# Performance work log

Measured on AMD Instinct MI355X. Metric: run time of the kernel, lower is better.

## Reference

```python
import jax, jax.numpy as jnp
import numpy as np

N, T0, T1, C = 65536, 128, 64, 16
MIN_NEAR = 0.05


def _searchsorted(a, v):
    # batched right-side searchsorted over last dim
    return jax.vmap(lambda aa, vv: jnp.searchsorted(aa, vv, side='right'))(a, v)


def contract(x):
    # MERF-style contraction, x: [..., 3]
    ax = jnp.abs(x)
    mag = jnp.max(ax, axis=-1, keepdims=True)              # [..., 1]
    idx = jnp.argmax(ax, axis=-1)                          # [...]
    oh = jnp.arange(x.shape[-1]) == idx[..., None]         # one-hot of max axis
    inv = 1.0 / mag
    scale = jnp.where(oh, (2.0 - inv) * inv, inv)
    return jnp.where(mag < 1.0, x, x * scale)


def sample_pdf(bins, weights, T):
    # bins: [N, T0+1], weights: [N, T0] -> new bins [N, T]
    n, t0 = weights.shape
    w = weights + 0.01
    pdf = w / jnp.sum(w, -1, keepdims=True)
    cdf = jnp.minimum(jnp.cumsum(pdf, -1), 1.0)
    cdf = jnp.concatenate([jnp.zeros_like(cdf[..., :1]), cdf], -1)  # [N, T0+1]
    u = jnp.linspace(0.5 / T, 1.0 - 0.5 / T, T, dtype=bins.dtype)
    u = jnp.broadcast_to(u, (n, T))
    inds = _searchsorted(cdf, u)
    below = jnp.clip(inds - 1, 0, t0)
    above = jnp.clip(inds, 0, t0)
    g = lambda a, i: jnp.take_along_axis(a, i, axis=-1)
    cdf0, cdf1 = g(cdf, below), g(cdf, above)
    b0, b1 = g(bins, below), g(bins, above)
    t = jnp.clip(jnp.nan_to_num((u - cdf0) / (cdf1 - cdf0)), 0.0, 1.0)
    return b0 + t * (b1 - b0)


def compute_weights(real_bins, sigmas):
    deltas = real_bins[..., 1:] - real_bins[..., :-1]
    ds = deltas * sigmas
    alphas = 1.0 - jnp.exp(-ds)
    trans = jnp.exp(-jnp.concatenate(
        [jnp.zeros_like(ds[..., :1]), jnp.cumsum(ds[..., :-1], -1)], -1))
    return jnp.nan_to_num(alphas * trans)


def loss_interlevel(t0, w0, t1, w1):
    cw1 = jnp.concatenate([jnp.zeros_like(w1[..., :1]), jnp.cumsum(w1, -1)], -1)
    hi_clip = w1.shape[-1] - 1
    inds_lo = jnp.clip(_searchsorted(t1[..., :-1], t0[..., :-1]) - 1, 0, hi_clip)
    inds_hi = jnp.clip(_searchsorted(t1[..., 1:], t0[..., 1:]), 0, hi_clip)
    cw1_lo = jnp.take_along_axis(cw1[..., :-1], inds_lo, axis=-1)
    cw1_hi = jnp.take_along_axis(cw1[..., 1:], inds_hi, axis=-1)
    w = cw1_hi - cw1_lo
    return jnp.maximum(w0 - w, 0.0) ** 2 / (w0 + 1e-8)


def eff_distloss(w, m, interval):
    # efficient O(T) distortion loss (torch_efficient_distloss)
    loss_uni = (1.0 / 3.0) * jnp.mean(jnp.sum(interval * w ** 2, -1))
    wm = w * m
    w_cs = jnp.cumsum(w, -1)
    wm_cs = jnp.cumsum(wm, -1)
    loss_bi = 2.0 * jnp.mean(jnp.sum(
        wm[..., 1:] * w_cs[..., :-1] - w[..., 1:] * wm_cs[..., :-1], -1))
    return loss_uni + loss_bi


def setup_inputs():
    key = jax.random.key(0)
    ks = jax.random.split(key, 8)
    rays_o = 0.1 * jax.random.normal(ks[0], (N, 3), jnp.float32)
    rd = jax.random.normal(ks[1], (N, 3), jnp.float32)
    rays_d = rd / jnp.linalg.norm(rd, axis=-1, keepdims=True)
    aabb = jnp.array([-2.0, -2.0, -2.0, 2.0, 2.0, 2.0], jnp.float32)
    sigmas_coarse = 5.0 * jax.random.uniform(ks[2], (N, T0), jnp.float32)
    sigmas_fine = 5.0 * jax.random.uniform(ks[3], (N, T1), jnp.float32)
    colors = jax.random.uniform(ks[4], (N, T1, C), jnp.float32)
    w_view = 0.1 * jax.random.normal(ks[5], (C, 3), jnp.float32)
    b_view = jnp.zeros((3,), jnp.float32)
    return dict(rays_o=rays_o, rays_d=rays_d, aabb=aabb,
                sigmas_coarse=sigmas_coarse, sigmas_fine=sigmas_fine,
                colors=colors, w_view=w_view, b_view=b_view)


def reference(rays_o, rays_d, aabb, sigmas_coarse, sigmas_fine, colors, w_view, b_view):
    # near/far from aabb
    tmin = (aabb[:3] - rays_o) / (rays_d + 1e-15)
    tmax = (aabb[3:] - rays_o) / (rays_d + 1e-15)
    near = jnp.max(jnp.minimum(tmin, tmax), -1, keepdims=True)
    far = jnp.min(jnp.maximum(tmin, tmax), -1, keepdims=True)
    bad = far < near
    near = jnp.maximum(jnp.where(bad, 1e9, near), MIN_NEAR)
    far = jnp.where(bad, 1e9, far)

    spacing = lambda x: jnp.where(x < 1.0, x / 2.0, 1.0 - 1.0 / (2.0 * x))
    spacing_inv = lambda x: jnp.where(x < 0.5, 2.0 * x, 1.0 / (2.0 - 2.0 * x))
    s_near, s_far = spacing(near), spacing(far)

    # coarse (proposal) level: uniform bins in warped space
    bins0 = jnp.broadcast_to(jnp.linspace(0.0, 1.0, T0 + 1, dtype=rays_o.dtype), (N, T0 + 1))
    real_bins0 = spacing_inv(s_near * (1.0 - bins0) + s_far * bins0)
    weights0 = compute_weights(real_bins0, sigmas_coarse)

    # fine level: inverse-CDF sampling (detached in original)
    bins1 = sample_pdf(jax.lax.stop_gradient(bins0),
                       jax.lax.stop_gradient(weights0), T1 + 1)
    real_bins1 = spacing_inv(s_near * (1.0 - bins1) + s_far * bins1)
    rays_t = 0.5 * (real_bins1[..., 1:] + real_bins1[..., :-1])      # [N, T1]
    xyzs = rays_o[:, None, :] + rays_d[:, None, :] * rays_t[..., None]
    xyzs = contract(xyzs)                                            # [N, T1, 3]
    weights1 = compute_weights(real_bins1, sigmas_fine)

    weights_sum = jnp.sum(weights1, -1)                              # [N]
    depth = jnp.sum(weights1 * rays_t, -1)                           # [N]
    f_image = jnp.sum(weights1[..., None] * colors, -2)              # [N, C]
    image = jax.nn.sigmoid(f_image @ w_view + b_view)                # [N, 3]
    image = image + (1.0 - weights_sum)[:, None] * 1.0               # bg_color = 1
    f_xyz = jnp.sum(weights1[..., None] * xyzs, -2)                  # [N, 3]

    prop_loss = jnp.mean(loss_interlevel(
        jax.lax.stop_gradient(bins1), jax.lax.stop_gradient(weights1),
        bins0, weights0))
    intervals = bins1[..., 1:] - bins1[..., :-1]
    mids = bins1[..., :-1] + intervals / 2.0
    dist_loss = eff_distloss(weights1, mids, intervals)

    return image, depth, f_xyz, prop_loss, dist_loss
```

## Files before the change

kernel.cpp:

```cpp
#include <hip/hip_runtime.h>
#include <math.h>

#define NRAYS 65536
#define T0N 128
#define T1N 64
#define CN 16
#define RPB 4
#define NBLK (NRAYS / RPB)

#define IMG_OFF   0
#define DEPTH_OFF (NRAYS * 3)
#define FXYZ_OFF  (NRAYS * 4)
#define PROP_OFF  (NRAYS * 7)
#define DIST_OFF  (NRAYS * 7 + 1)

__device__ __forceinline__ float frcp(float x) { return __builtin_amdgcn_rcpf(x); }

template <int CTRL, int RM, int BM, bool BC>
__device__ __forceinline__ float dpp_add(float x) {
  int t = __builtin_amdgcn_update_dpp(0, __float_as_int(x), CTRL, RM, BM, BC);
  return x + __int_as_float(t);
}

__device__ __forceinline__ float scan_incl(float x) {
  x = dpp_add<0x111, 0xF, 0xF, true>(x);
  x = dpp_add<0x112, 0xF, 0xF, true>(x);
  x = dpp_add<0x114, 0xF, 0xF, true>(x);
  x = dpp_add<0x118, 0xF, 0xF, true>(x);
  x = dpp_add<0x142, 0xA, 0xF, false>(x);
  x = dpp_add<0x143, 0xC, 0xF, false>(x);
  return x;
}

__device__ __forceinline__ float reduce_hi(float x) {
  x = dpp_add<0xB1, 0xF, 0xF, true>(x);
  x = dpp_add<0x4E, 0xF, 0xF, true>(x);
  x = dpp_add<0x141, 0xF, 0xF, true>(x);
  x = dpp_add<0x140, 0xF, 0xF, true>(x);
  x = dpp_add<0x142, 0xA, 0xF, false>(x);
  x = dpp_add<0x143, 0xC, 0xF, false>(x);
  return x;
}

__device__ __forceinline__ float rl63(float x) {
  return __int_as_float(__builtin_amdgcn_readlane(__float_as_int(x), 63));
}

__device__ __forceinline__ void wave_lds_sync() {
  __builtin_amdgcn_wave_barrier();
  __builtin_amdgcn_fence(__ATOMIC_ACQ_REL, "workgroup");
  __builtin_amdgcn_wave_barrier();
}

__device__ __forceinline__ float spacing_fn(float x) {
  return (x < 1.0f) ? (x * 0.5f) : (1.0f - 0.5f * frcp(x));
}
__device__ __forceinline__ float spacing_inv_fn(float x) {
  return (x < 0.5f) ? (2.0f * x) : frcp(2.0f - 2.0f * x);
}

template <int W0>
__device__ __forceinline__ int count_le(const float* a, float v) {
  int pos = 0;
#pragma unroll
  for (int w = W0; w > 0; w >>= 1) pos += (a[pos + w - 1] <= v) ? w : 0;
  return pos;
}

__global__ void __launch_bounds__(256) nerf_main(
    const float* __restrict__ rays_o, const float* __restrict__ rays_d,
    const float* __restrict__ aabb, const float* __restrict__ sig_c,
    const float* __restrict__ sig_f, const float* __restrict__ colors,
    const float* __restrict__ w_view, const float* __restrict__ b_view,
    float* __restrict__ out, float* __restrict__ ws_partials, int use_atomic) {
  __shared__ float s_cdf[RPB][224];
  __shared__ float s_bins1[RPB][129];
  __shared__ float s_cw1[RPB][65];
  __shared__ float s_scal[RPB][2];

  const int wv = threadIdx.x >> 6;
  const int lane = threadIdx.x & 63;
  const int ray = blockIdx.x * RPB + wv;

  const int tg = lane >> 2, cg = lane & 3;
  const float4* col4 = (const float4*)(colors + (size_t)ray * (T1N * CN));
  const float4 cva = col4[(tg + 0) * 4 + cg];
  const float4 cvb = col4[(tg + 16) * 4 + cg];
  const float4 cvc = col4[(tg + 32) * 4 + cg];
  const float4 cvd = col4[(tg + 48) * 4 + cg];
  const float2 sg = ((const float2*)sig_c)[ray * 64 + lane];
  const float sgf = sig_f[ray * 64 + lane];

  float ro[3], rd[3];
#pragma unroll
  for (int c = 0; c < 3; ++c) { ro[c] = rays_o[ray * 3 + c]; rd[c] = rays_d[ray * 3 + c]; }
  float near = -3.0e38f, far = 3.0e38f;
#pragma unroll
  for (int c = 0; c < 3; ++c) {
    const float rdd = frcp(rd[c] + 1e-15f);
    float ta = (aabb[c] - ro[c]) * rdd;
    float tb = (aabb[c + 3] - ro[c]) * rdd;
    near = fmaxf(near, fminf(ta, tb));
    far = fminf(far, fmaxf(ta, tb));
  }
  if (far < near) { near = 1e9f; far = 1e9f; }
  near = fmaxf(near, 0.05f);
  const float s_near = spacing_fn(near), s_far = spacing_fn(far);

  const int i0 = 2 * lane, i1 = 2 * lane + 1;
  const float b_a = (float)i0 * (1.0f / 128.0f);
  const float b_b = (float)i1 * (1.0f / 128.0f);
  const float b_c = (float)(i1 + 1) * (1.0f / 128.0f);
  const float rb_a = spacing_inv_fn(s_near * (1.0f - b_a) + s_far * b_a);
  const float rb_b = spacing_inv_fn(s_near * (1.0f - b_b) + s_far * b_b);
  const float rb_c = spacing_inv_fn(s_near * (1.0f - b_c) + s_far * b_c);
  const float ds0 = (rb_b - rb_a) * sg.x;
  const float ds1 = (rb_c - rb_b) * sg.y;
  const float Spr = scan_incl(ds0 + ds1);
  const float E0 = Spr - (ds0 + ds1);
  const float e0 = __expf(-E0);
  const float ed0 = __expf(-ds0);
  float w00 = (1.0f - ed0) * e0;
  float w01 = (1.0f - __expf(-ds1)) * (e0 * ed0);
  if (w00 != w00) w00 = 0.0f;
  if (w01 != w01) w01 = 0.0f;

  const float wp0 = w00 + 0.01f, wp1 = w01 + 0.01f;
  const float S2 = scan_incl(wp0 + wp1);
  const float rt = frcp(rl63(S2));
  s_cdf[wv][i0 + 1] = fminf((S2 - wp1) * rt, 1.0f);
  s_cdf[wv][i1 + 1] = fminf(S2 * rt, 1.0f);
  if (lane == 0) s_cdf[wv][0] = 0.0f;
  s_cdf[wv][129 + lane] = 2.0f;
  wave_lds_sync();

  auto sample_one = [&](int j) -> float {
    const float u = ((float)j + 0.5f) * (1.0f / 65.0f);
    const int c = count_le<128>(&s_cdf[wv][0], u);
    const float c0 = s_cdf[wv][c - 1], c1 = s_cdf[wv][c];
    const float b0 = (float)(c - 1) * (1.0f / 128.0f);
    float t = (u - c0) * frcp(c1 - c0);
    t = fminf(fmaxf(t, 0.0f), 1.0f);
    const float bvv = b0 + t * (1.0f / 128.0f);
    s_bins1[wv][j] = bvv;
    return bvv;
  };
  const float bv = sample_one(lane);
  float bv64 = 0.0f;
  if (lane == 63) bv64 = sample_one(64);
  s_bins1[wv][65 + lane] = 2.0f;
  float bvn = __shfl_down(bv, 1, 64);
  if (lane == 63) bvn = bv64;

  const float rbl  = spacing_inv_fn(s_near * (1.0f - bv)  + s_far * bv);
  const float rbl1 = spacing_inv_fn(s_near * (1.0f - bvn) + s_far * bvn);
  const float dsf = (rbl1 - rbl) * sgf;
  const float Sf = scan_incl(dsf);
  float w1 = (1.0f - __expf(-dsf)) * __expf(-(Sf - dsf));
  if (w1 != w1) w1 = 0.0f;
  const float tmid = 0.5f * (rbl + rbl1);

  float px = ro[0] + rd[0] * tmid;
  float py = ro[1] + rd[1] * tmid;
  float pz = ro[2] + rd[2] * tmid;
  float cx = px, cy = py, cz = pz;
  {
    float ax = fabsf(px), ay = fabsf(py), az = fabsf(pz);
    float mag = fmaxf(ax, fmaxf(ay, az));
    if (mag >= 1.0f) {
      float inv = frcp(mag);
      float so = (2.0f - inv) * inv;
      int idx = (ax >= ay && ax >= az) ? 0 : ((ay >= az) ? 1 : 2);
      cx = px * (idx == 0 ? so : inv);
      cy = py * (idx == 1 ? so : inv);
      cz = pz * (idx == 2 ? so : inv);
    }
  }

  const float Scw = scan_incl(w1);
  const float wsum = rl63(Scw);
  const float depth_h = reduce_hi(w1 * tmid);
  const float fx_h = reduce_hi(w1 * cx);
  const float fy_h = reduce_hi(w1 * cy);
  const float fz_h = reduce_hi(w1 * cz);
  s_cw1[wv][lane + 1] = Scw;
  if (lane == 0) s_cw1[wv][0] = 0.0f;

  const float interval = bvn - bv;
  const float mid = bv + interval * 0.5f;
  const float wm = w1 * mid;
  const float Swm = scan_incl(wm);
  const float dl = (1.0f / 3.0f) * (interval * w1 * w1) +
                   2.0f * (wm * (Scw - w1) - w1 * (Swm - wm));
  const float dist_h = reduce_hi(dl);
  wave_lds_sync();

  float prop_lane = 0.0f;
  {
    const float* b1p = &s_bins1[wv][0];
    const float* cwp = &s_cw1[wv][0];
#pragma unroll
    for (int k = 0; k < 2; ++k) {
      int i = 2 * lane + k;
      float w0v = (k == 0) ? w00 : w01;
      float vlo = (float)i * (1.0f / 128.0f);
      float vhi = (float)(i + 1) * (1.0f / 128.0f);
      int ilo = max(min(count_le<64>(b1p, vlo) - 1, 63), 0);
      int ihi = min(count_le<64>(b1p + 1, vhi), 63);
      float wint = cwp[ihi + 1] - cwp[ilo];
      float diff = fmaxf(w0v - wint, 0.0f);
      prop_lane += diff * diff * frcp(w0v + 1e-8f);
    }
  }
  const float prop_h = reduce_hi(prop_lane);

  float acc0, acc1, acc2;
  {
    const float wv0 = __shfl(w1, tg, 64);
    const float wv1 = __shfl(w1, tg + 16, 64);
    const float wv2 = __shfl(w1, tg + 32, 64);
    const float wv3 = __shfl(w1, tg + 48, 64);
    const float a0 = fmaf(wv0, cva.x, fmaf(wv1, cvb.x, fmaf(wv2, cvc.x, wv3 * cvd.x)));
    const float a1 = fmaf(wv0, cva.y, fmaf(wv1, cvb.y, fmaf(wv2, cvc.y, wv3 * cvd.y)));
    const float a2 = fmaf(wv0, cva.z, fmaf(wv1, cvb.z, fmaf(wv2, cvc.z, wv3 * cvd.z)));
    const float a3 = fmaf(wv0, cva.w, fmaf(wv1, cvb.w, fmaf(wv2, cvc.w, wv3 * cvd.w)));
    const float* wvp = w_view + cg * 12;
    acc0 = reduce_hi(fmaf(a0, wvp[0], fmaf(a1, wvp[3], fmaf(a2, wvp[6], a3 * wvp[9]))));
    acc1 = reduce_hi(fmaf(a0, wvp[1], fmaf(a1, wvp[4], fmaf(a2, wvp[7], a3 * wvp[10]))));
    acc2 = reduce_hi(fmaf(a0, wvp[2], fmaf(a1, wvp[5], fmaf(a2, wvp[8], a3 * wvp[11]))));
  }

  if (lane >= 48 && lane < 51) {
    const int j = lane - 48;
    float acc = (j == 0) ? acc0 : ((j == 1) ? acc1 : acc2);
    acc += b_view[j];
    out[IMG_OFF + ray * 3 + j] = frcp(1.0f + __expf(-acc)) + (1.0f - wsum);
    out[FXYZ_OFF + ray * 3 + j] = (j == 0) ? fx_h : ((j == 1) ? fy_h : fz_h);
  }
  if (lane == 51) out[DEPTH_OFF + ray] = depth_h;
  if (lane == 52) { s_scal[wv][0] = prop_h; s_scal[wv][1] = dist_h; }
  __syncthreads();
  if (threadIdx.x == 0) {
    float P = s_scal[0][0] + s_scal[1][0] + s_scal[2][0] + s_scal[3][0];
    float D = s_scal[0][1] + s_scal[1][1] + s_scal[2][1] + s_scal[3][1];
    if (use_atomic) {
      atomicAdd(out + PROP_OFF, P * (1.0f / ((float)NRAYS * 128.0f)));
      atomicAdd(out + DIST_OFF, D * (1.0f / (float)NRAYS));
    } else {
      ws_partials[blockIdx.x] = P;
      ws_partials[NBLK + blockIdx.x] = D;
    }
  }
}

__device__ __forceinline__ float wave_sum_shfl(float x) {
#pragma unroll
  for (int off = 1; off < 64; off <<= 1) x += __shfl_xor(x, off, 64);
  return x;
}

__global__ void __launch_bounds__(256) reduce_partials(const float* __restrict__ ws,
                                                       float* __restrict__ out) {
  const float4* w4 = (const float4*)ws;
  float p = 0.0f, d = 0.0f;
  for (int i = threadIdx.x; i < NBLK / 4; i += 256) {
    float4 a = w4[i];
    p += (a.x + a.y) + (a.z + a.w);
    float4 b = w4[NBLK / 4 + i];
    d += (b.x + b.y) + (b.z + b.w);
  }
  p = wave_sum_shfl(p);
  d = wave_sum_shfl(d);
  __shared__ float sp[4], sd[4];
  const int wv = threadIdx.x >> 6, lane = threadIdx.x & 63;
  if (lane == 0) { sp[wv] = p; sd[wv] = d; }
  __syncthreads();
  if (threadIdx.x == 0) {
    float P = sp[0] + sp[1] + sp[2] + sp[3];
    float D = sd[0] + sd[1] + sd[2] + sd[3];
    out[PROP_OFF] = P * (1.0f / ((float)NRAYS * 128.0f));
    out[DIST_OFF] = D * (1.0f / (float)NRAYS);
  }
}

extern "C" void kernel_launch(void* const* d_in, const int* in_sizes, int n_in,
                              void* d_out, int out_size, void* d_ws, size_t ws_size,
                              hipStream_t stream) {
  const float* rays_o = (const float*)d_in[0];
  const float* rays_d = (const float*)d_in[1];
  const float* aabb = (const float*)d_in[2];
  const float* sig_c = (const float*)d_in[3];
  const float* sig_f = (const float*)d_in[4];
  const float* colors = (const float*)d_in[5];
  const float* w_view = (const float*)d_in[6];
  const float* b_view = (const float*)d_in[7];
  float* out = (float*)d_out;
  float* wsf = (float*)d_ws;

  const bool use_ws = (ws_size >= (size_t)(2 * NBLK) * sizeof(float)) && (wsf != nullptr);
  if (!use_ws) {
    hipMemsetAsync(out + PROP_OFF, 0, 2 * sizeof(float), stream);
  }
  nerf_main<<<NBLK, 256, 0, stream>>>(rays_o, rays_d, aabb, sig_c, sig_f, colors,
                                      w_view, b_view, out, wsf, use_ws ? 0 : 1);
  if (use_ws) reduce_partials<<<1, 256, 0, stream>>>(wsf, out);
}
```

Before: 409.0 us.

## Replace binary-search searchsorted with LDS histogram counting and prefix scans

Replaces the per-lane binary searches over the CDF and the fine bins with scatter-add counting into LDS histograms, then uses wave prefix scans to recover the searchsorted indices. This removes the serial dependent LDS loads of each binary search in both the PDF sampling and the interlevel loss. In exchange it adds LDS atomics, zero-initialisation of a larger shared buffer, and index derivation through float ceil, which may differ from the reference at exact boundaries. It also hoists the w_view and b_view loads to the top of the kernel and widens the final reduction kernel to 1024 threads.

```diff
diff --git a/kernel.cpp b/kernel.cpp
--- a/kernel.cpp
+++ b/kernel.cpp
@@ -59,12 +59,8 @@
   return (x < 0.5f) ? (2.0f * x) : frcp(2.0f - 2.0f * x);
 }
 
-template <int W0>
-__device__ __forceinline__ int count_le(const float* a, float v) {
-  int pos = 0;
-#pragma unroll
-  for (int w = W0; w > 0; w >>= 1) pos += (a[pos + w - 1] <= v) ? w : 0;
-  return pos;
+__device__ __forceinline__ int clampi(int v, int lo, int hi) {
+  return min(max(v, lo), hi);
 }
 
 __global__ void __launch_bounds__(256) nerf_main(
@@ -73,14 +69,21 @@
     const float* __restrict__ sig_f, const float* __restrict__ colors,
     const float* __restrict__ w_view, const float* __restrict__ b_view,
     float* __restrict__ out, float* __restrict__ ws_partials, int use_atomic) {
-  __shared__ float s_cdf[RPB][224];
-  __shared__ float s_bins1[RPB][129];
+  __shared__ float s_cdf[RPB][132];
+  __shared__ __align__(16) float s_dif[RPB][400];
   __shared__ float s_cw1[RPB][65];
   __shared__ float s_scal[RPB][2];
 
   const int wv = threadIdx.x >> 6;
   const int lane = threadIdx.x & 63;
   const int ray = blockIdx.x * RPB + wv;
+
+  {
+    float4 z4 = make_float4(0.0f, 0.0f, 0.0f, 0.0f);
+    float4* zp = (float4*)&s_dif[wv][0];
+    zp[lane] = z4;
+    if (lane < 36) zp[64 + lane] = z4;
+  }
 
   const int tg = lane >> 2, cg = lane & 3;
   const float4* col4 = (const float4*)(colors + (size_t)ray * (T1N * CN));
@@ -90,6 +93,10 @@
   const float4 cvd = col4[(tg + 48) * 4 + cg];
   const float2 sg = ((const float2*)sig_c)[ray * 64 + lane];
   const float sgf = sig_f[ray * 64 + lane];
+  const float4 wv4a = *(const float4*)(w_view + cg * 12);
+  const float4 wv4b = *(const float4*)(w_view + cg * 12 + 4);
+  const float4 wv4c = *(const float4*)(w_view + cg * 12 + 8);
+  const float bpre = b_view[clampi(lane - 48, 0, 2)];
 
   float ro[3], rd[3];
 #pragma unroll
@@ -128,29 +135,51 @@
   const float wp0 = w00 + 0.01f, wp1 = w01 + 0.01f;
   const float S2 = scan_incl(wp0 + wp1);
   const float rt = frcp(rl63(S2));
-  s_cdf[wv][i0 + 1] = fminf((S2 - wp1) * rt, 1.0f);
-  s_cdf[wv][i1 + 1] = fminf(S2 * rt, 1.0f);
+  const float cdfA = fminf((S2 - wp1) * rt, 1.0f);
+  const float cdfB = fminf(S2 * rt, 1.0f);
+  s_cdf[wv][i0 + 1] = cdfA;
+  s_cdf[wv][i1 + 1] = cdfB;
   if (lane == 0) s_cdf[wv][0] = 0.0f;
-  s_cdf[wv][129 + lane] = 2.0f;
+  if (lane < 3) s_cdf[wv][129 + lane] = 2.0f;
+
+  {
+    float* dS = &s_dif[wv][0];
+    const int KA = clampi((int)ceilf(fmaf(65.0f, cdfA, -0.5f)), 0, 65);
+    const int KB = clampi((int)ceilf(fmaf(65.0f, cdfB, -0.5f)), 0, 65);
+    atomicAdd(&dS[KA], 1.0f);
+    atomicAdd(&dS[KB], 1.0f);
+  }
   wave_lds_sync();
 
-  auto sample_one = [&](int j) -> float {
-    const float u = ((float)j + 0.5f) * (1.0f / 65.0f);
-    const int c = count_le<128>(&s_cdf[wv][0], u);
-    const float c0 = s_cdf[wv][c - 1], c1 = s_cdf[wv][c];
-    const float b0 = (float)(c - 1) * (1.0f / 128.0f);
-    float t = (u - c0) * frcp(c1 - c0);
-    t = fminf(fmaxf(t, 0.0f), 1.0f);
-    const float bvv = b0 + t * (1.0f / 128.0f);
-    s_bins1[wv][j] = bvv;
-    return bvv;
-  };
-  const float bv = sample_one(lane);
-  float bv64 = 0.0f;
-  if (lane == 63) bv64 = sample_one(64);
-  s_bins1[wv][65 + lane] = 2.0f;
+  const float* dS = &s_dif[wv][0];
+  const float dme = dS[lane];
+  const float Ps = scan_incl(dme);
+  const float d64 = dS[64];
+  const int c = 1 + (int)Ps;
+  const float c0 = s_cdf[wv][c - 1], c1 = s_cdf[wv][c];
+  const float u = ((float)lane + 0.5f) * (1.0f / 65.0f);
+  float t = (u - c0) * frcp(c1 - c0);
+  t = fminf(fmaxf(t, 0.0f), 1.0f);
+  const float b0f = (float)(c - 1) * (1.0f / 128.0f);
+  const float bv = fmaf(t, 1.0f / 128.0f, b0f);
+  const int c64 = 1 + (int)(rl63(Ps) + d64);
+  const float C0 = s_cdf[wv][c64 - 1], C1 = s_cdf[wv][c64];
+  const float u64v = 64.5f * (1.0f / 65.0f);
+  float t64 = (u64v - C0) * frcp(C1 - C0);
+  t64 = fminf(fmaxf(t64, 0.0f), 1.0f);
+  const float bv64 = fmaf(t64, 1.0f / 128.0f, (float)(c64 - 1) * (1.0f / 128.0f));
   float bvn = __shfl_down(bv, 1, 64);
   if (lane == 63) bvn = bv64;
+
+  {
+    float* dLo = &s_dif[wv][68];
+    float* dHi = &s_dif[wv][200];
+    const int KL = clampi((int)ceilf(128.0f * bv), 0, 128);
+    atomicAdd(&dLo[KL], 1.0f);
+    const float bH = (lane == 0) ? bv64 : bv;
+    const int KH = clampi((int)ceilf(128.0f * bH) - 1, 0, 128);
+    atomicAdd(&dHi[KH], 1.0f);
+  }
 
   const float rbl  = spacing_inv_fn(s_near * (1.0f - bv)  + s_far * bv);
   const float rbl1 = spacing_inv_fn(s_near * (1.0f - bvn) + s_far * bvn);
@@ -195,45 +224,44 @@
   const float dist_h = reduce_hi(dl);
   wave_lds_sync();
 
-  float prop_lane = 0.0f;
-  {
-    const float* b1p = &s_bins1[wv][0];
+  float prop_lane;
+  {
     const float* cwp = &s_cw1[wv][0];
-#pragma unroll
-    for (int k = 0; k < 2; ++k) {
-      int i = 2 * lane + k;
-      float w0v = (k == 0) ? w00 : w01;
-      float vlo = (float)i * (1.0f / 128.0f);
-      float vhi = (float)(i + 1) * (1.0f / 128.0f);
-      int ilo = max(min(count_le<64>(b1p, vlo) - 1, 63), 0);
-      int ihi = min(count_le<64>(b1p + 1, vhi), 63);
-      float wint = cwp[ihi + 1] - cwp[ilo];
-      float diff = fmaxf(w0v - wint, 0.0f);
-      prop_lane += diff * diff * frcp(w0v + 1e-8f);
-    }
+    const float2 dL = ((const float2*)&s_dif[wv][68])[lane];
+    const float2 dH = ((const float2*)&s_dif[wv][200])[lane];
+    const float sL = scan_incl(dL.x + dL.y);
+    const float sH = scan_incl(dH.x + dH.y);
+    const int iloA = clampi((int)(sL - dL.y) - 1, 0, 63);
+    const int iloB = clampi((int)sL - 1, 0, 63);
+    const int ihiA = min((int)(sH - dH.y), 63);
+    const int ihiB = min((int)sH, 63);
+    const float wA = cwp[ihiA + 1] - cwp[iloA];
+    const float wB = cwp[ihiB + 1] - cwp[iloB];
+    const float dA = fmaxf(w00 - wA, 0.0f);
+    const float dB = fmaxf(w01 - wB, 0.0f);
+    prop_lane = dA * dA * frcp(w00 + 1e-8f) + dB * dB * frcp(w01 + 1e-8f);
   }
   const float prop_h = reduce_hi(prop_lane);
 
   float acc0, acc1, acc2;
   {
-    const float wv0 = __shfl(w1, tg, 64);
-    const float wv1 = __shfl(w1, tg + 16, 64);
-    const float wv2 = __shfl(w1, tg + 32, 64);
-    const float wv3 = __shfl(w1, tg + 48, 64);
-    const float a0 = fmaf(wv0, cva.x, fmaf(wv1, cvb.x, fmaf(wv2, cvc.x, wv3 * cvd.x)));
-    const float a1 = fmaf(wv0, cva.y, fmaf(wv1, cvb.y, fmaf(wv2, cvc.y, wv3 * cvd.y)));
-    const float a2 = fmaf(wv0, cva.z, fmaf(wv1, cvb.z, fmaf(wv2, cvc.z, wv3 * cvd.z)));
-    const float a3 = fmaf(wv0, cva.w, fmaf(wv1, cvb.w, fmaf(wv2, cvc.w, wv3 * cvd.w)));
-    const float* wvp = w_view + cg * 12;
-    acc0 = reduce_hi(fmaf(a0, wvp[0], fmaf(a1, wvp[3], fmaf(a2, wvp[6], a3 * wvp[9]))));
-    acc1 = reduce_hi(fmaf(a0, wvp[1], fmaf(a1, wvp[4], fmaf(a2, wvp[7], a3 * wvp[10]))));
-    acc2 = reduce_hi(fmaf(a0, wvp[2], fmaf(a1, wvp[5], fmaf(a2, wvp[8], a3 * wvp[11]))));
+    const float wvv0 = __shfl(w1, tg, 64);
+    const float wvv1 = __shfl(w1, tg + 16, 64);
+    const float wvv2 = __shfl(w1, tg + 32, 64);
+    const float wvv3 = __shfl(w1, tg + 48, 64);
+    const float a0 = fmaf(wvv0, cva.x, fmaf(wvv1, cvb.x, fmaf(wvv2, cvc.x, wvv3 * cvd.x)));
+    const float a1 = fmaf(wvv0, cva.y, fmaf(wvv1, cvb.y, fmaf(wvv2, cvc.y, wvv3 * cvd.y)));
+    const float a2 = fmaf(wvv0, cva.z, fmaf(wvv1, cvb.z, fmaf(wvv2, cvc.z, wvv3 * cvd.z)));
+    const float a3 = fmaf(wvv0, cva.w, fmaf(wvv1, cvb.w, fmaf(wvv2, cvc.w, wvv3 * cvd.w)));
+    acc0 = reduce_hi(fmaf(a0, wv4a.x, fmaf(a1, wv4a.w, fmaf(a2, wv4b.z, a3 * wv4c.y))));
+    acc1 = reduce_hi(fmaf(a0, wv4a.y, fmaf(a1, wv4b.x, fmaf(a2, wv4b.w, a3 * wv4c.z))));
+    acc2 = reduce_hi(fmaf(a0, wv4a.z, fmaf(a1, wv4b.y, fmaf(a2, wv4c.x, a3 * wv4c.w))));
   }
 
   if (lane >= 48 && lane < 51) {
     const int j = lane - 48;
     float acc = (j == 0) ? acc0 : ((j == 1) ? acc1 : acc2);
-    acc += b_view[j];
+    acc += bpre;
     out[IMG_OFF + ray * 3 + j] = frcp(1.0f + __expf(-acc)) + (1.0f - wsum);
     out[FXYZ_OFF + ray * 3 + j] = (j == 0) ? fx_h : ((j == 1) ? fy_h : fz_h);
   }
@@ -259,11 +287,11 @@
   return x;
 }
 
-__global__ void __launch_bounds__(256) reduce_partials(const float* __restrict__ ws,
-                                                       float* __restrict__ out) {
+__global__ void __launch_bounds__(1024) reduce_partials(const float* __restrict__ ws,
+                                                        float* __restrict__ out) {
   const float4* w4 = (const float4*)ws;
   float p = 0.0f, d = 0.0f;
-  for (int i = threadIdx.x; i < NBLK / 4; i += 256) {
+  for (int i = threadIdx.x; i < NBLK / 4; i += 1024) {
     float4 a = w4[i];
     p += (a.x + a.y) + (a.z + a.w);
     float4 b = w4[NBLK / 4 + i];
@@ -271,13 +299,14 @@
   }
   p = wave_sum_shfl(p);
   d = wave_sum_shfl(d);
-  __shared__ float sp[4], sd[4];
+  __shared__ float sp[16], sd[16];
   const int wv = threadIdx.x >> 6, lane = threadIdx.x & 63;
   if (lane == 0) { sp[wv] = p; sd[wv] = d; }
   __syncthreads();
   if (threadIdx.x == 0) {
-    float P = sp[0] + sp[1] + sp[2] + sp[3];
-    float D = sd[0] + sd[1] + sd[2] + sd[3];
+    float P = 0.0f, D = 0.0f;
+#pragma unroll
+    for (int k = 0; k < 16; ++k) { P += sp[k]; D += sd[k]; }
     out[PROP_OFF] = P * (1.0f / ((float)NRAYS * 128.0f));
     out[DIST_OFF] = D * (1.0f / (float)NRAYS);
   }
@@ -303,5 +332,5 @@
   }
   nerf_main<<<NBLK, 256, 0, stream>>>(rays_o, rays_d, aabb, sig_c, sig_f, colors,
                                       w_view, b_view, out, wsf, use_ws ? 0 : 1);
-  if (use_ws) reduce_partials<<<1, 256, 0, stream>>>(wsf, out);
-}
+  if (use_ws) reduce_partials<<<1, 1024, 0, stream>>>(wsf, out);
+}
```

Result: no change. 412.6 us (+0.9%).
